# Performance work log

Hardware: AMD Instinct MI355X
Metric: run time of the kernel (lower is better)

## Reference

```python
import jax, jax.numpy as jnp
import numpy as np

D_MODEL = 1024
D_STATE = 16
LN_EPS = 1e-5


def setup_inputs() -> dict:
    key = jax.random.key(0)
    ks = jax.random.split(key, 10)
    B, L, D, N = 4, 1024, D_MODEL, D_STATE
    s = lambda fan_in: 1.0 / np.sqrt(fan_in)
    x_in = jax.random.normal(ks[0], (B, L, D), dtype=jnp.float32)
    W_in = jax.random.uniform(ks[1], (D, 2 * D), jnp.float32, -s(D), s(D))
    W_x = jax.random.uniform(ks[2], (D, D + 2 * N), jnp.float32, -s(D), s(D))
    W_dt = jax.random.uniform(ks[3], (D, D), jnp.float32, -s(D), s(D))
    b_dt = jax.random.uniform(ks[4], (D,), jnp.float32, -4.0, -1.0)
    A_log = jnp.tile(jnp.log(jnp.arange(1, N + 1, dtype=jnp.float32))[None, :], (D, 1))
    D_param = jnp.ones((D,), dtype=jnp.float32)
    W_out = jax.random.uniform(ks[5], (D, D), jnp.float32, -s(D), s(D))
    ln_g = jnp.ones((D,), dtype=jnp.float32)
    ln_b = jnp.zeros((D,), dtype=jnp.float32)
    return {"x_in": x_in, "W_in": W_in, "W_x": W_x, "W_dt": W_dt, "b_dt": b_dt,
            "A_log": A_log, "D_param": D_param, "W_out": W_out, "ln_g": ln_g, "ln_b": ln_b}


def reference(x_in, W_in, W_x, W_dt, b_dt, A_log, D_param, W_out, ln_g, ln_b):
    B, L, D = x_in.shape
    N = A_log.shape[1]
    xz = x_in @ W_in                       # [B,L,2D]
    x, z = xz[..., :D], xz[..., D:]
    proj = x @ W_x                         # [B,L,D+2N]
    delta_raw = proj[..., :D]
    B_ssm = proj[..., D:D + N]
    C_ssm = proj[..., D + N:]
    delta = jax.nn.softplus(delta_raw @ W_dt + b_dt)   # [B,L,D]
    A = -jnp.exp(A_log)                    # [D,N]
    dA = jnp.exp(jnp.einsum('bld,dn->bldn', delta, A))      # [B,L,D,N]
    dBx = jnp.einsum('bld,bln->bldn', delta * x, B_ssm)      # dB * x, fused

    def step(h, inp):
        dA_t, dBx_t, C_t = inp             # [B,D,N],[B,D,N],[B,N]
        h = dA_t * h + dBx_t
        y_t = jnp.einsum('bdn,bn->bd', h, C_t)
        return h, y_t

    h0 = jnp.zeros((B, D, N), dtype=x.dtype)
    xs = (jnp.moveaxis(dA, 1, 0), jnp.moveaxis(dBx, 1, 0), jnp.moveaxis(C_ssm, 1, 0))
    _, ys = jax.lax.scan(step, h0, xs)     # ys: [L,B,D]
    y = jnp.moveaxis(ys, 0, 1) + x * D_param
    y = (y * jax.nn.silu(z)) @ W_out
    res = y + x_in
    mu = jnp.mean(res, axis=-1, keepdims=True)
    var = jnp.var(res, axis=-1, keepdims=True)
    return (res - mu) * jax.lax.rsqrt(var + LN_EPS) * ln_g + ln_b
```

## Files before the change

kernel.cpp:

```cpp
#include <hip/hip_runtime.h>

#define D_MODEL 1024
#define D_STATE 16
#define M_ROWS  4096
#define SEQ_L   1024
#define NSEG    32
#define LSEG    32

typedef __bf16 bf16x8 __attribute__((ext_vector_type(8)));
typedef float  f32x4  __attribute__((ext_vector_type(4)));

__device__ __forceinline__ unsigned short f2bf(float f) {
  unsigned int u = __builtin_bit_cast(unsigned int, f);
  u += 0x7fffu + ((u >> 16) & 1u);
  return (unsigned short)(u >> 16);
}
__device__ __forceinline__ float bf2f(unsigned short b) {
  unsigned int u = ((unsigned int)b) << 16;
  return __builtin_bit_cast(float, u);
}
__device__ __forceinline__ float load_elem(const void* p, size_t i, int isbf) {
  if (isbf) return bf2f(((const unsigned short*)p)[i]);
  return ((const float*)p)[i];
}

__device__ __forceinline__ void gload16(const void* g, void* l) {
  typedef const __attribute__((address_space(1))) unsigned int GU;
  typedef __attribute__((address_space(3))) unsigned int LU;
  __builtin_amdgcn_global_load_lds((GU*)(unsigned long long)g,
                                   (LU*)(unsigned int)(unsigned long long)l,
                                   16, 0, 0);
}

__global__ void detect_kernel(const unsigned short* __restrict__ x, int* __restrict__ flag) {
  __shared__ int cnt;
  if (threadIdx.x == 0) cnt = 0;
  __syncthreads();
  unsigned int v = x[2 * threadIdx.x];
  unsigned int e = (v >> 7) & 0xFFu;
  int ok = (e >= 100u && e <= 135u) ? 1 : 0;
  atomicAdd(&cnt, ok);
  __syncthreads();
  if (threadIdx.x == 0) *flag = (cnt >= 128) ? 1 : 0;
}

__global__ void convert_x_kernel(const void* __restrict__ src, float* __restrict__ dstf,
                                 unsigned short* __restrict__ dstb,
                                 const int* __restrict__ flag) {
  int c = blockIdx.x * blockDim.x + threadIdx.x;
  int isbf = *flag;
  float o[8];
  if (isbf) {
    uint4 v = ((const uint4*)src)[c];
    o[0] = bf2f((unsigned short)(v.x & 0xffffu)); o[1] = bf2f((unsigned short)(v.x >> 16));
    o[2] = bf2f((unsigned short)(v.y & 0xffffu)); o[3] = bf2f((unsigned short)(v.y >> 16));
    o[4] = bf2f((unsigned short)(v.z & 0xffffu)); o[5] = bf2f((unsigned short)(v.z >> 16));
    o[6] = bf2f((unsigned short)(v.w & 0xffffu)); o[7] = bf2f((unsigned short)(v.w >> 16));
    ((uint4*)dstb)[c] = v;
  } else {
    float4 a = ((const float4*)src)[2 * c];
    float4 b = ((const float4*)src)[2 * c + 1];
    o[0]=a.x; o[1]=a.y; o[2]=a.z; o[3]=a.w; o[4]=b.x; o[5]=b.y; o[6]=b.z; o[7]=b.w;
    uint4 p;
    p.x = (unsigned int)f2bf(o[0]) | ((unsigned int)f2bf(o[1]) << 16);
    p.y = (unsigned int)f2bf(o[2]) | ((unsigned int)f2bf(o[3]) << 16);
    p.z = (unsigned int)f2bf(o[4]) | ((unsigned int)f2bf(o[5]) << 16);
    p.w = (unsigned int)f2bf(o[6]) | ((unsigned int)f2bf(o[7]) << 16);
    ((uint4*)dstb)[c] = p;
  }
  float4* d = (float4*)dstf;
  d[2*c]   = make_float4(o[0], o[1], o[2], o[3]);
  d[2*c+1] = make_float4(o[4], o[5], o[6], o[7]);
}

__global__ void convert_raw_kernel(const void* __restrict__ src, unsigned short* __restrict__ dst,
                                   const int* __restrict__ flag) {
  int c = blockIdx.x * blockDim.x + threadIdx.x;
  int isbf = *flag;
  if (isbf) {
    ((uint4*)dst)[c] = ((const uint4*)src)[c];
  } else {
    float4 a = ((const float4*)src)[2 * c];
    float4 b = ((const float4*)src)[2 * c + 1];
    uint4 p;
    p.x = (unsigned int)f2bf(a.x) | ((unsigned int)f2bf(a.y) << 16);
    p.y = (unsigned int)f2bf(a.z) | ((unsigned int)f2bf(a.w) << 16);
    p.z = (unsigned int)f2bf(b.x) | ((unsigned int)f2bf(b.y) << 16);
    p.w = (unsigned int)f2bf(b.z) | ((unsigned int)f2bf(b.w) << 16);
    ((uint4*)dst)[c] = p;
  }
}

__global__ void convert_smalls_kernel(const void* b_dt, const void* A_log, const void* Dp,
                                      const void* ln_g, const void* ln_b,
                                      float* o_bdt, float* o_a2, float* o_dp,
                                      float* o_lng, float* o_lnb,
                                      const int* __restrict__ flag) {
  int g = blockIdx.x * blockDim.x + threadIdx.x;
  int isbf = *flag;
  if (g < 1024)              o_bdt[g]          = load_elem(b_dt, g, isbf);
  else if (g < 17408) {
    float v = load_elem(A_log, g - 1024, isbf);
    o_a2[g - 1024] = -expf(v) * 1.4426950408889634f;
  }
  else if (g < 18432)        o_dp[g - 17408]   = load_elem(Dp, g - 17408, isbf);
  else if (g < 19456)        o_lng[g - 18432]  = load_elem(ln_g, g - 18432, isbf);
  else                       o_lnb[g - 19456]  = load_elem(ln_b, g - 19456, isbf);
}

__global__ void transpose_w_kernel(const void* __restrict__ src, unsigned short* __restrict__ dst,
                                   int ncols, int col0, const int* __restrict__ flag) {
  __shared__ float tile[32][33];
  int tx = threadIdx.x, ty = threadIdx.y;
  int n0 = col0 + blockIdx.x * 32, k0 = blockIdx.y * 32;
  int isbf = *flag;
  #pragma unroll
  for (int r = 0; r < 4; ++r) {
    int k = k0 + ty + r * 8;
    int n = n0 + tx;
    float v = (n < ncols) ? load_elem(src, (size_t)k * ncols + n, isbf) : 0.f;
    tile[ty + r * 8][tx] = v;
  }
  __syncthreads();
  #pragma unroll
  for (int r = 0; r < 4; ++r) {
    int n = n0 + ty + r * 8;
    int k = k0 + tx;
    dst[(size_t)(n - col0) * 1024 + k] = f2bf(tile[tx][ty + r * 8]);
  }
}

template<int MODE>
__global__ __launch_bounds__(256, 3) void gemm_bf(
    const unsigned short* __restrict__ A, const unsigned short* __restrict__ Bt, int ldb,
    void* __restrict__ o0, void* __restrict__ o1, void* __restrict__ o2,
    float* __restrict__ o3, float* __restrict__ o4,
    const float* __restrict__ aux) {
  constexpr int NITER = D_MODEL / 32;
  __shared__ __align__(16) unsigned short a_lds[3][128 * 32];
  __shared__ __align__(16) unsigned short b_lds[3][128 * 32];
  const int tid = threadIdx.x;
  const int m0 = blockIdx.x * 128, n0 = blockIdx.y * 128;
  const int wave = tid >> 6, lane = tid & 63;
  const int wr = (wave >> 1) * 64, wc = (wave & 1) * 64;
  const int lrow = lane & 15, quad = lane >> 4;

  const int srow = wave * 32 + (lane >> 2);
  const int sc = (lane & 3) ^ ((lane >> 3) & 3);
  const unsigned short* gA  = A  + (size_t)(m0 + srow) * 1024 + sc * 8;
  const unsigned short* gA2 = gA + 16 * 1024;
  const unsigned short* gB  = Bt + (size_t)(n0 + srow) * ldb + sc * 8;
  const unsigned short* gB2 = gB + (size_t)16 * ldb;
  const int soff = wave * 32 * 32;

  const int q2 = quad ^ ((lrow >> 1) & 3);

  f32x4 acc[4][4];
  #pragma unroll
  for (int i = 0; i < 4; ++i)
    #pragma unroll
    for (int jj = 0; jj < 4; ++jj)
      #pragma unroll
      for (int r = 0; r < 4; ++r) acc[i][jj][r] = 0.f;

  auto issue = [&](int k) {
    unsigned short* ab = &a_lds[k % 3][soff];
    unsigned short* bb = &b_lds[k % 3][soff];
    gload16(gA  + k * 32, ab);
    gload16(gA2 + k * 32, ab + 16 * 32);
    gload16(gB  + k * 32, bb);
    gload16(gB2 + k * 32, bb + 16 * 32);
  };
  auto compute = [&](int k) {
    const unsigned short* ard = &a_lds[k % 3][(wr + lrow) * 32 + q2 * 8];
    const unsigned short* brd = &b_lds[k % 3][(wc + lrow) * 32 + q2 * 8];
    bf16x8 af[4], bfr[4];
    #pragma unroll
    for (int i = 0; i < 4; ++i) {
      af[i]  = *(const bf16x8*)(ard + i * 16 * 32);
      bfr[i] = *(const bf16x8*)(brd + i * 16 * 32);
    }
    #pragma unroll
    for (int i = 0; i < 4; ++i)
      #pragma unroll
      for (int jj = 0; jj < 4; ++jj)
        acc[i][jj] = __builtin_amdgcn_mfma_f32_16x16x32_bf16(af[i], bfr[jj], acc[i][jj], 0, 0, 0);
  };

  issue(0);
  issue(1);
  #pragma unroll
  for (int k = 0; k < NITER - 1; ++k) {
    asm volatile("s_waitcnt vmcnt(4)" ::: "memory");
    __builtin_amdgcn_s_barrier();
    if (k + 2 < NITER) issue(k + 2);
    compute(k);
  }
  asm volatile("s_waitcnt vmcnt(0)" ::: "memory");
  __builtin_amdgcn_s_barrier();
  compute(NITER - 1);

  #pragma unroll
  for (int i = 0; i < 4; ++i) {
    #pragma unroll
    for (int jj = 0; jj < 4; ++jj) {
      #pragma unroll
      for (int r = 0; r < 4; ++r) {
        int m = m0 + wr + i * 16 + quad * 4 + r;
        int n = n0 + wc + jj * 16 + lrow;
        float v = acc[i][jj][r];
        if (MODE == 0) {
          ((unsigned short*)o0)[(size_t)m * 1024 + n] = f2bf(v);
        } else if (MODE == 1) {
          if (n < 1024) {
            ((unsigned short*)o0)[(size_t)m * 1024 + n] = f2bf(v);
          } else if (n < 2048) {
            float sig = 1.f / (1.f + expf(-v));
            ((unsigned short*)o1)[(size_t)m * 1024 + (n - 1024)] = f2bf(v * sig);
          } else if (n < 3072) {
            float t = v + aux[n - 2048];
            float sp = (t > 20.f) ? t : log1pf(expf(t));
            ((unsigned short*)o2)[(size_t)m * 1024 + (n - 2048)] = f2bf(sp);
          } else if (n < 3088) {
            o3[(size_t)m * D_STATE + (n - 3072)] = v;
          } else if (n < 3104) {
            o4[(size_t)m * D_STATE + (n - 3088)] = v;
          }
        } else {
          ((float*)o0)[(size_t)m * 1024 + n] = v + aux[(size_t)m * 1024 + n];
        }
      }
    }
  }
}

template<int PHASE>
__global__ __launch_bounds__(256) void scan_phase(
    const unsigned short* __restrict__ dl_bf, const unsigned short* __restrict__ x_bf,
    const unsigned short* __restrict__ z_bf, const float* __restrict__ Bs,
    const float* __restrict__ Cs, const float* __restrict__ A2g,
    const float* __restrict__ Dpar, const float* __restrict__ hinit,
    float* __restrict__ Hout, float* __restrict__ sdout,
    unsigned short* __restrict__ g) {
  __shared__ float4 bsh[LSEG][4];
  __shared__ float4 csh[LSEG][4];
  const int tid = threadIdx.x;
  const int bid = blockIdx.x;
  const int seg = bid >> 4;
  const int b = (bid >> 2) & 3;
  const int dc = bid & 3;
  const int d = dc * 256 + tid;
  const int t0 = seg * LSEG;
  const int bd = b * D_MODEL + d;

  if (tid < 128) {
    int r = tid >> 2, q = tid & 3;
    size_t src = ((size_t)b * SEQ_L + t0 + r) * 4 + q;
    bsh[r][q] = ((const float4*)Bs)[src];
    if (PHASE == 1) csh[r][q] = ((const float4*)Cs)[src];
  }

  float A2r[16];
  {
    const float4* a4 = (const float4*)(A2g + (size_t)d * 16);
    #pragma unroll
    for (int q = 0; q < 4; ++q) {
      float4 v = a4[q];
      A2r[4*q] = v.x; A2r[4*q+1] = v.y; A2r[4*q+2] = v.z; A2r[4*q+3] = v.w;
    }
  }
  float h[16];
  if (PHASE == 1) {
    const float4* h4 = (const float4*)(hinit + (((size_t)seg * 4096) + bd) * 16);
    #pragma unroll
    for (int q = 0; q < 4; ++q) {
      float4 v = h4[q];
      h[4*q] = v.x; h[4*q+1] = v.y; h[4*q+2] = v.z; h[4*q+3] = v.w;
    }
  } else {
    #pragma unroll
    for (int n = 0; n < 16; ++n) h[n] = 0.f;
  }
  const float Dpd = (PHASE == 1) ? Dpar[d] : 0.f;
  float sd = 0.f;
  const size_t base = ((size_t)b * SEQ_L + t0) * D_MODEL + d;
  __syncthreads();

  unsigned short dreg[2][8], xreg[2][8], zreg[2][8];
  #pragma unroll
  for (int t = 0; t < 8; ++t) {
    size_t o = base + (size_t)t * D_MODEL;
    dreg[0][t] = dl_bf[o]; xreg[0][t] = x_bf[o];
    if (PHASE == 1) zreg[0][t] = z_bf[o];
  }
  #pragma unroll
  for (int c = 0; c < LSEG / 8; ++c) {
    const int cur = c & 1, nxt = cur ^ 1;
    if (c < LSEG / 8 - 1) {
      #pragma unroll
      for (int t = 0; t < 8; ++t) {
        size_t o = base + (size_t)((c + 1) * 8 + t) * D_MODEL;
        dreg[nxt][t] = dl_bf[o]; xreg[nxt][t] = x_bf[o];
        if (PHASE == 1) zreg[nxt][t] = z_bf[o];
      }
    }
    #pragma unroll
    for (int t = 0; t < 8; ++t) {
      const int tt = c * 8 + t;
      float dl = bf2f(dreg[cur][t]);
      float xx = bf2f(xreg[cur][t]);
      float dx = dl * xx;
      sd += dl;
      float4 b0 = bsh[tt][0], b1 = bsh[tt][1], b2 = bsh[tt][2], b3 = bsh[tt][3];
      float bb[16] = {b0.x,b0.y,b0.z,b0.w, b1.x,b1.y,b1.z,b1.w,
                      b2.x,b2.y,b2.z,b2.w, b3.x,b3.y,b3.z,b3.w};
      if (PHASE == 0) {
        #pragma unroll
        for (int n = 0; n < 16; ++n) {
          float dA = exp2f(dl * A2r[n]);
          h[n] = fmaf(dA, h[n], dx * bb[n]);
        }
      } else {
        float4 c0 = csh[tt][0], c1 = csh[tt][1], c2 = csh[tt][2], c3 = csh[tt][3];
        float cc[16] = {c0.x,c0.y,c0.z,c0.w, c1.x,c1.y,c1.z,c1.w,
                        c2.x,c2.y,c2.z,c2.w, c3.x,c3.y,c3.z,c3.w};
        float y = 0.f;
        #pragma unroll
        for (int n = 0; n < 16; ++n) {
          float dA = exp2f(dl * A2r[n]);
          h[n] = fmaf(dA, h[n], dx * bb[n]);
          y = fmaf(h[n], cc[n], y);
        }
        float zz = bf2f(zreg[cur][t]);
        g[base + (size_t)tt * D_MODEL] = f2bf(fmaf(xx, Dpd, y) * zz);
      }
    }
  }
  if (PHASE == 0) {
    float4* ho = (float4*)(Hout + (((size_t)seg * 4096) + bd) * 16);
    #pragma unroll
    for (int q = 0; q < 4; ++q)
      ho[q] = make_float4(h[4*q], h[4*q+1], h[4*q+2], h[4*q+3]);
    sdout[(size_t)seg * 4096 + bd] = sd;
  }
}

__global__ __launch_bounds__(256) void scan_phaseB(
    const float* __restrict__ H, const float* __restrict__ sdelta,
    const float* __restrict__ A2g, float* __restrict__ hinit) {
  int gidx = blockIdx.x * 256 + threadIdx.x;
  int bd = gidx >> 4, n = gidx & 15;
  float A2 = A2g[(size_t)(bd & (D_MODEL - 1)) * 16 + n];
  float hp = 0.f;
  #pragma unroll
  for (int s = 0; s < NSEG; ++s) {
    size_t idx = ((size_t)s * 4096 + bd) * 16 + n;
    hinit[idx] = hp;
    float P = exp2f(A2 * sdelta[(size_t)s * 4096 + bd]);
    hp = fmaf(P, hp, H[idx]);
  }
}

__global__ __launch_bounds__(256) void ln_kernel(const float* __restrict__ res,
    const float* __restrict__ lng, const float* __restrict__ lnb,
    void* __restrict__ out, const int* __restrict__ flag) {
  int row = blockIdx.x, tid = threadIdx.x;
  const float4* r4 = (const float4*)(res + (size_t)row * D_MODEL);
  float4 v = r4[tid];
  float s = v.x + v.y + v.z + v.w;
  float q = v.x * v.x + v.y * v.y + v.z * v.z + v.w * v.w;
  #pragma unroll
  for (int m = 1; m < 64; m <<= 1) { s += __shfl_xor(s, m); q += __shfl_xor(q, m); }
  __shared__ float ss[4], qs[4];
  int w = tid >> 6;
  if ((tid & 63) == 0) { ss[w] = s; qs[w] = q; }
  __syncthreads();
  s = ss[0] + ss[1] + ss[2] + ss[3];
  q = qs[0] + qs[1] + qs[2] + qs[3];
  float mu = s * (1.f / D_MODEL);
  float var = q * (1.f / D_MODEL) - mu * mu;
  float rstd = rsqrtf(var + 1e-5f);
  float4 gg = ((const float4*)lng)[tid];
  float4 bb = ((const float4*)lnb)[tid];
  float o0 = (v.x - mu) * rstd * gg.x + bb.x;
  float o1 = (v.y - mu) * rstd * gg.y + bb.y;
  float o2 = (v.z - mu) * rstd * gg.z + bb.z;
  float o3 = (v.w - mu) * rstd * gg.w + bb.w;
  if (*flag) {
    ushort4 pv;
    pv.x = f2bf(o0); pv.y = f2bf(o1); pv.z = f2bf(o2); pv.w = f2bf(o3);
    ((ushort4*)out)[(size_t)row * 256 + tid] = pv;
  } else {
    ((float4*)out)[(size_t)row * 256 + tid] = make_float4(o0, o1, o2, o3);
  }
}

extern "C" void kernel_launch(void* const* d_in, const int* in_sizes, int n_in,
                              void* d_out, int out_size, void* d_ws, size_t ws_size,
                              hipStream_t stream) {
  (void)in_sizes; (void)n_in; (void)out_size; (void)ws_size;
  const void* x_in  = d_in[0];
  const void* W_in  = d_in[1];
  const void* W_x   = d_in[2];
  const void* W_dt  = d_in[3];
  const void* b_dt  = d_in[4];
  const void* A_log = d_in[5];
  const void* D_par = d_in[6];
  const void* W_out = d_in[7];
  const void* ln_g  = d_in[8];
  const void* ln_b  = d_in[9];

  char* ws = (char*)d_ws;
  size_t off = 0;
  auto alloc = [&](size_t bytes) -> void* {
    void* p = ws + off;
    off += (bytes + 255) & ~(size_t)255;
    return p;
  };
  int* flag              = (int*)alloc(16);
  float* x_in_f          = (float*)alloc((size_t)M_ROWS * D_MODEL * 4);
  unsigned short* x_in_b = (unsigned short*)alloc((size_t)M_ROWS * D_MODEL * 2);
  float* bdt_f           = (float*)alloc(1024 * 4);
  float* a2_f            = (float*)alloc(16384 * 4);
  float* dp_f            = (float*)alloc(1024 * 4);
  float* lng_f           = (float*)alloc(1024 * 4);
  float* lnb_f           = (float*)alloc(1024 * 4);
  unsigned short* win_raw= (unsigned short*)alloc((size_t)1024 * 2048 * 2);
  unsigned short* wx_raw = (unsigned short*)alloc((size_t)1024 * 1056 * 2);
  unsigned short* wt_dt  = (unsigned short*)alloc((size_t)1024 * 1024 * 2);
  unsigned short* wt_out = (unsigned short*)alloc((size_t)1024 * 1024 * 2);
  unsigned short* wt_xbc = (unsigned short*)alloc((size_t)128 * 1024 * 2);
  unsigned short* U_bf   = (unsigned short*)alloc((size_t)1024 * 1024 * 2);
  unsigned short* btbig  = (unsigned short*)alloc((size_t)3200 * 1024 * 2);
  unsigned short* x_bf   = (unsigned short*)alloc((size_t)M_ROWS * D_MODEL * 2);
  unsigned short* s_bf   = (unsigned short*)alloc((size_t)M_ROWS * D_MODEL * 2);
  unsigned short* delta_bf=(unsigned short*)alloc((size_t)M_ROWS * D_MODEL * 2);
  float* bssm_f          = (float*)alloc((size_t)M_ROWS * D_STATE * 4);
  float* cssm_f          = (float*)alloc((size_t)M_ROWS * D_STATE * 4);
  float* H_f             = (float*)alloc((size_t)NSEG * 4096 * 16 * 4);
  float* hinit_f         = (float*)alloc((size_t)NSEG * 4096 * 16 * 4);
  float* sdelta_f        = (float*)alloc((size_t)NSEG * 4096 * 4);
  unsigned short* g_bf   = (unsigned short*)alloc((size_t)M_ROWS * D_MODEL * 2);
  float* res_f = (float*)x_bf;

  detect_kernel<<<1, 256, 0, stream>>>((const unsigned short*)x_in, flag);
  convert_x_kernel<<<2048, 256, 0, stream>>>(x_in, x_in_f, x_in_b, flag);
  convert_smalls_kernel<<<80, 256, 0, stream>>>(b_dt, A_log, D_par, ln_g, ln_b,
                                                bdt_f, a2_f, dp_f, lng_f, lnb_f, flag);
  convert_raw_kernel<<<1024, 256, 0, stream>>>(W_in, win_raw, flag);
  convert_raw_kernel<<<528, 256, 0, stream>>>(W_x, wx_raw, flag);
  dim3 tb(32, 8);
  transpose_w_kernel<<<dim3(64, 32), tb, 0, stream>>>(W_in,  btbig,  2048, 0, flag);
  transpose_w_kernel<<<dim3(4, 32),  tb, 0, stream>>>(W_x,   wt_xbc, 1056, 1024, flag);
  transpose_w_kernel<<<dim3(32, 32), tb, 0, stream>>>(W_dt,  wt_dt,  1024, 0, flag);
  transpose_w_kernel<<<dim3(32, 32), tb, 0, stream>>>(W_out, wt_out, 1024, 0, flag);

  gemm_bf<0><<<dim3(8, 8), 256, 0, stream>>>(wt_dt, wx_raw, 1056, U_bf,
                                             nullptr, nullptr, nullptr, nullptr, nullptr);
  gemm_bf<0><<<dim3(8, 8), 256, 0, stream>>>(U_bf, win_raw, 2048, btbig + (size_t)2048 * 1024,
                                             nullptr, nullptr, nullptr, nullptr, nullptr);
  gemm_bf<0><<<dim3(1, 8), 256, 0, stream>>>(wt_xbc, win_raw, 2048, btbig + (size_t)3072 * 1024,
                                             nullptr, nullptr, nullptr, nullptr, nullptr);

  gemm_bf<1><<<dim3(32, 25), 256, 0, stream>>>(x_in_b, btbig, 1024,
                                               x_bf, s_bf, delta_bf, bssm_f, cssm_f, bdt_f);

  scan_phase<0><<<512, 256, 0, stream>>>(delta_bf, x_bf, nullptr, bssm_f, nullptr,
                                         a2_f, nullptr, nullptr, H_f, sdelta_f, nullptr);
  scan_phaseB<<<256, 256, 0, stream>>>(H_f, sdelta_f, a2_f, hinit_f);
  scan_phase<1><<<512, 256, 0, stream>>>(delta_bf, x_bf, s_bf, bssm_f, cssm_f,
                                         a2_f, dp_f, hinit_f, nullptr, nullptr, g_bf);

  gemm_bf<4><<<dim3(32, 8), 256, 0, stream>>>(g_bf, wt_out, 1024,
                                              res_f, nullptr, nullptr, nullptr, nullptr, x_in_f);
  ln_kernel<<<4096, 256, 0, stream>>>(res_f, lng_f, lnb_f, d_out, flag);
}
```

Before: 303.2 us.

## Enlarge GEMM tiles to 256x128 and merge weight-prep kernel launches

The bf16 MFMA GEMM now uses a 256x128 block tile with 8x4 accumulators per wave, a triple-buffered A and double-buffered B in LDS, and launch bounds lowered from 3 to 2 blocks per CU. The aim is more reuse of the B tile per global load. Separately, the two weight-convert launches and four transpose launches are each merged into one kernel. The two small weight-product GEMMs are folded into one MODE 5 launch that switches on blockIdx to reduce launch overhead. The cost is half as many blocks per GEMM, so the output projection has fewer blocks than CUs. The merged small GEMM also reads and writes a 256-row tile for a 128-row operand, so a larger scratch buffer is allocated.

```diff
diff --git a/kernel.cpp b/kernel.cpp
--- a/kernel.cpp
+++ b/kernel.cpp
@@ -73,9 +73,13 @@
   d[2*c+1] = make_float4(o[4], o[5], o[6], o[7]);
 }
 
-__global__ void convert_raw_kernel(const void* __restrict__ src, unsigned short* __restrict__ dst,
-                                   const int* __restrict__ flag) {
+__global__ void convert_w_kernel(const void* __restrict__ w_in, const void* __restrict__ w_x,
+                                 unsigned short* __restrict__ d_in, unsigned short* __restrict__ d_x,
+                                 const int* __restrict__ flag) {
   int c = blockIdx.x * blockDim.x + threadIdx.x;
+  const void* src; unsigned short* dst;
+  if (c < 262144) { src = w_in; dst = d_in; }
+  else { c -= 262144; if (c >= 135168) return; src = w_x; dst = d_x; }
   int isbf = *flag;
   if (isbf) {
     ((uint4*)dst)[c] = ((const uint4*)src)[c];
@@ -108,9 +112,20 @@
   else                       o_lnb[g - 19456]  = load_elem(ln_b, g - 19456, isbf);
 }
 
-__global__ void transpose_w_kernel(const void* __restrict__ src, unsigned short* __restrict__ dst,
-                                   int ncols, int col0, const int* __restrict__ flag) {
+__global__ void transpose_all_kernel(const void* __restrict__ s0, const void* __restrict__ s1,
+                                     const void* __restrict__ s2, const void* __restrict__ s3,
+                                     unsigned short* __restrict__ d0, unsigned short* __restrict__ d1,
+                                     unsigned short* __restrict__ d2, unsigned short* __restrict__ d3,
+                                     const int* __restrict__ flag) {
   __shared__ float tile[32][33];
+  const void* src; unsigned short* dst; int ncols, col0, nx;
+  switch (blockIdx.z) {
+    case 0:  src = s0; dst = d0; ncols = 2048; col0 = 0;    nx = 64; break;
+    case 1:  src = s1; dst = d1; ncols = 1056; col0 = 1024; nx = 4;  break;
+    case 2:  src = s2; dst = d2; ncols = 1024; col0 = 0;    nx = 32; break;
+    default: src = s3; dst = d3; ncols = 1024; col0 = 0;    nx = 32; break;
+  }
+  if ((int)blockIdx.x >= nx) return;
   int tx = threadIdx.x, ty = threadIdx.y;
   int n0 = col0 + blockIdx.x * 32, k0 = blockIdx.y * 32;
   int isbf = *flag;
@@ -131,77 +146,82 @@
 }
 
 template<int MODE>
-__global__ __launch_bounds__(256, 3) void gemm_bf(
-    const unsigned short* __restrict__ A, const unsigned short* __restrict__ Bt, int ldb,
+__global__ __launch_bounds__(256, 2) void gemm_bf(
+    const unsigned short* __restrict__ A, const unsigned short* __restrict__ A2,
+    const unsigned short* __restrict__ Bt, int ldb,
     void* __restrict__ o0, void* __restrict__ o1, void* __restrict__ o2,
     float* __restrict__ o3, float* __restrict__ o4,
     const float* __restrict__ aux) {
-  constexpr int NITER = D_MODEL / 32;
-  __shared__ __align__(16) unsigned short a_lds[3][128 * 32];
-  __shared__ __align__(16) unsigned short b_lds[3][128 * 32];
+  __shared__ __align__(16) unsigned short a_lds[3][256 * 32];
+  __shared__ __align__(16) unsigned short b_lds[2][128 * 32];
   const int tid = threadIdx.x;
-  const int m0 = blockIdx.x * 128, n0 = blockIdx.y * 128;
+  int m0 = blockIdx.x * 256;
+  const int n0 = blockIdx.y * 128;
+  const unsigned short* Ap = A;
+  if (MODE == 5 && blockIdx.x == 4) { Ap = A2; m0 = 0; }
   const int wave = tid >> 6, lane = tid & 63;
-  const int wr = (wave >> 1) * 64, wc = (wave & 1) * 64;
+  const int wr = (wave >> 1) * 128, wc = (wave & 1) * 64;
   const int lrow = lane & 15, quad = lane >> 4;
 
-  const int srow = wave * 32 + (lane >> 2);
+  const int arow = wave * 64 + (lane >> 2);
+  const int brow = wave * 32 + (lane >> 2);
   const int sc = (lane & 3) ^ ((lane >> 3) & 3);
-  const unsigned short* gA  = A  + (size_t)(m0 + srow) * 1024 + sc * 8;
-  const unsigned short* gA2 = gA + 16 * 1024;
-  const unsigned short* gB  = Bt + (size_t)(n0 + srow) * ldb + sc * 8;
-  const unsigned short* gB2 = gB + (size_t)16 * ldb;
-  const int soff = wave * 32 * 32;
-
+  const unsigned short* gA = Ap + (size_t)(m0 + arow) * 1024 + sc * 8;
+  const unsigned short* gB = Bt + (size_t)(n0 + brow) * ldb + sc * 8;
+  const int aoff = wave * 64 * 32;
+  const int boff = wave * 32 * 32;
   const int q2 = quad ^ ((lrow >> 1) & 3);
 
-  f32x4 acc[4][4];
-  #pragma unroll
-  for (int i = 0; i < 4; ++i)
+  f32x4 acc[8][4];
+  #pragma unroll
+  for (int i = 0; i < 8; ++i)
     #pragma unroll
     for (int jj = 0; jj < 4; ++jj)
       #pragma unroll
       for (int r = 0; r < 4; ++r) acc[i][jj][r] = 0.f;
 
-  auto issue = [&](int k) {
-    unsigned short* ab = &a_lds[k % 3][soff];
-    unsigned short* bb = &b_lds[k % 3][soff];
-    gload16(gA  + k * 32, ab);
-    gload16(gA2 + k * 32, ab + 16 * 32);
-    gload16(gB  + k * 32, bb);
-    gload16(gB2 + k * 32, bb + 16 * 32);
+  auto issueA = [&](int k) {
+    unsigned short* d = a_lds[k % 3] + aoff;
+    gload16(gA + k * 32,             d);
+    gload16(gA + k * 32 + 16 * 1024, d + 16 * 32);
+    gload16(gA + k * 32 + 32 * 1024, d + 32 * 32);
+    gload16(gA + k * 32 + 48 * 1024, d + 48 * 32);
+  };
+  auto issueB = [&](int k) {
+    unsigned short* d = b_lds[k % 2] + boff;
+    gload16(gB + k * 32,                    d);
+    gload16(gB + (size_t)16 * ldb + k * 32, d + 16 * 32);
   };
   auto compute = [&](int k) {
-    const unsigned short* ard = &a_lds[k % 3][(wr + lrow) * 32 + q2 * 8];
-    const unsigned short* brd = &b_lds[k % 3][(wc + lrow) * 32 + q2 * 8];
-    bf16x8 af[4], bfr[4];
-    #pragma unroll
-    for (int i = 0; i < 4; ++i) {
-      af[i]  = *(const bf16x8*)(ard + i * 16 * 32);
-      bfr[i] = *(const bf16x8*)(brd + i * 16 * 32);
-    }
-    #pragma unroll
-    for (int i = 0; i < 4; ++i)
+    const unsigned short* ard = a_lds[k % 3] + (wr + lrow) * 32 + q2 * 8;
+    const unsigned short* brd = b_lds[k % 2] + (wc + lrow) * 32 + q2 * 8;
+    bf16x8 af[8], bfr[4];
+    #pragma unroll
+    for (int i = 0; i < 8; ++i) af[i] = *(const bf16x8*)(ard + i * 16 * 32);
+    #pragma unroll
+    for (int jj = 0; jj < 4; ++jj) bfr[jj] = *(const bf16x8*)(brd + jj * 16 * 32);
+    #pragma unroll
+    for (int i = 0; i < 8; ++i)
       #pragma unroll
       for (int jj = 0; jj < 4; ++jj)
         acc[i][jj] = __builtin_amdgcn_mfma_f32_16x16x32_bf16(af[i], bfr[jj], acc[i][jj], 0, 0, 0);
   };
 
-  issue(0);
-  issue(1);
-  #pragma unroll
-  for (int k = 0; k < NITER - 1; ++k) {
+  issueA(0); issueB(0); issueA(1);
+  #pragma unroll
+  for (int k = 0; k < 31; ++k) {
     asm volatile("s_waitcnt vmcnt(4)" ::: "memory");
     __builtin_amdgcn_s_barrier();
-    if (k + 2 < NITER) issue(k + 2);
+    issueB(k + 1);
+    if (k + 2 < 32) issueA(k + 2);
     compute(k);
   }
   asm volatile("s_waitcnt vmcnt(0)" ::: "memory");
   __builtin_amdgcn_s_barrier();
-  compute(NITER - 1);
-
-  #pragma unroll
-  for (int i = 0; i < 4; ++i) {
+  compute(31);
+
+  #pragma unroll
+  for (int i = 0; i < 8; ++i) {
     #pragma unroll
     for (int jj = 0; jj < 4; ++jj) {
       #pragma unroll
@@ -209,8 +229,10 @@
         int m = m0 + wr + i * 16 + quad * 4 + r;
         int n = n0 + wc + jj * 16 + lrow;
         float v = acc[i][jj][r];
-        if (MODE == 0) {
-          ((unsigned short*)o0)[(size_t)m * 1024 + n] = f2bf(v);
+        if (MODE == 0 || MODE == 5) {
+          unsigned short* dst = (unsigned short*)o0;
+          if (MODE == 5 && blockIdx.x == 4) dst = (unsigned short*)o1;
+          dst[(size_t)m * 1024 + n] = f2bf(v);
         } else if (MODE == 1) {
           if (n < 1024) {
             ((unsigned short*)o0)[(size_t)m * 1024 + n] = f2bf(v);
@@ -431,7 +453,7 @@
   unsigned short* wt_out = (unsigned short*)alloc((size_t)1024 * 1024 * 2);
   unsigned short* wt_xbc = (unsigned short*)alloc((size_t)128 * 1024 * 2);
   unsigned short* U_bf   = (unsigned short*)alloc((size_t)1024 * 1024 * 2);
-  unsigned short* btbig  = (unsigned short*)alloc((size_t)3200 * 1024 * 2);
+  unsigned short* btbig  = (unsigned short*)alloc((size_t)3328 * 1024 * 2);
   unsigned short* x_bf   = (unsigned short*)alloc((size_t)M_ROWS * D_MODEL * 2);
   unsigned short* s_bf   = (unsigned short*)alloc((size_t)M_ROWS * D_MODEL * 2);
   unsigned short* delta_bf=(unsigned short*)alloc((size_t)M_ROWS * D_MODEL * 2);
@@ -447,22 +469,19 @@
   convert_x_kernel<<<2048, 256, 0, stream>>>(x_in, x_in_f, x_in_b, flag);
   convert_smalls_kernel<<<80, 256, 0, stream>>>(b_dt, A_log, D_par, ln_g, ln_b,
                                                 bdt_f, a2_f, dp_f, lng_f, lnb_f, flag);
-  convert_raw_kernel<<<1024, 256, 0, stream>>>(W_in, win_raw, flag);
-  convert_raw_kernel<<<528, 256, 0, stream>>>(W_x, wx_raw, flag);
+  convert_w_kernel<<<1553, 256, 0, stream>>>(W_in, W_x, win_raw, wx_raw, flag);
   dim3 tb(32, 8);
-  transpose_w_kernel<<<dim3(64, 32), tb, 0, stream>>>(W_in,  btbig,  2048, 0, flag);
-  transpose_w_kernel<<<dim3(4, 32),  tb, 0, stream>>>(W_x,   wt_xbc, 1056, 1024, flag);
-  transpose_w_kernel<<<dim3(32, 32), tb, 0, stream>>>(W_dt,  wt_dt,  1024, 0, flag);
-  transpose_w_kernel<<<dim3(32, 32), tb, 0, stream>>>(W_out, wt_out, 1024, 0, flag);
-
-  gemm_bf<0><<<dim3(8, 8), 256, 0, stream>>>(wt_dt, wx_raw, 1056, U_bf,
+  transpose_all_kernel<<<dim3(64, 32, 4), tb, 0, stream>>>(
+      W_in, W_x, W_dt, W_out, btbig, wt_xbc, wt_dt, wt_out, flag);
+
+  gemm_bf<0><<<dim3(4, 8), 256, 0, stream>>>(wt_dt, nullptr, wx_raw, 1056, U_bf,
                                              nullptr, nullptr, nullptr, nullptr, nullptr);
-  gemm_bf<0><<<dim3(8, 8), 256, 0, stream>>>(U_bf, win_raw, 2048, btbig + (size_t)2048 * 1024,
-                                             nullptr, nullptr, nullptr, nullptr, nullptr);
-  gemm_bf<0><<<dim3(1, 8), 256, 0, stream>>>(wt_xbc, win_raw, 2048, btbig + (size_t)3072 * 1024,
-                                             nullptr, nullptr, nullptr, nullptr, nullptr);
-
-  gemm_bf<1><<<dim3(32, 25), 256, 0, stream>>>(x_in_b, btbig, 1024,
+  gemm_bf<5><<<dim3(5, 8), 256, 0, stream>>>(U_bf, wt_xbc, win_raw, 2048,
+                                             btbig + (size_t)2048 * 1024,
+                                             btbig + (size_t)3072 * 1024,
+                                             nullptr, nullptr, nullptr, nullptr);
+
+  gemm_bf<1><<<dim3(16, 25), 256, 0, stream>>>(x_in_b, nullptr, btbig, 1024,
                                                x_bf, s_bf, delta_bf, bssm_f, cssm_f, bdt_f);
 
   scan_phase<0><<<512, 256, 0, stream>>>(delta_bf, x_bf, nullptr, bssm_f, nullptr,
@@ -471,7 +490,7 @@
   scan_phase<1><<<512, 256, 0, stream>>>(delta_bf, x_bf, s_bf, bssm_f, cssm_f,
                                          a2_f, dp_f, hinit_f, nullptr, nullptr, g_bf);
 
-  gemm_bf<4><<<dim3(32, 8), 256, 0, stream>>>(g_bf, wt_out, 1024,
+  gemm_bf<4><<<dim3(16, 8), 256, 0, stream>>>(g_bf, nullptr, wt_out, 1024,
                                               res_f, nullptr, nullptr, nullptr, nullptr, x_in_f);
   ln_kernel<<<4096, 256, 0, stream>>>(res_f, lng_f, lnb_f, d_out, flag);
 }
```

After: 346.5 us. 14.3% more time.
